# Kernel optimization log

Hardware: AMD Instinct MI355X
Metric: run time of the kernel (lower is better)

The kernel has to match this reference:

```python
import jax, jax.numpy as jnp
import numpy as np

B, HQ, S, D = 2, 16, 2048, 64   # batch, query heads, seq len, head dim
DV = 2 * D                      # value head dim (differential attention)
LAMBDA_INIT = 0.8
EPS = 1e-5
NEG = -1.0e9


def setup_inputs() -> dict:
    key = jax.random.key(0)
    ks = jax.random.split(key, 8)
    return {
        "q": jax.random.normal(ks[0], (B, HQ, S, D), dtype=jnp.float32),
        "k": jax.random.normal(ks[1], (B, HQ, S, D), dtype=jnp.float32),
        "v": jax.random.normal(ks[2], (B, HQ // 2, S, DV), dtype=jnp.float32),
        "lambda_q1": jax.random.normal(ks[3], (D,), dtype=jnp.float32) * 0.1,
        "lambda_k1": jax.random.normal(ks[4], (D,), dtype=jnp.float32) * 0.1,
        "lambda_q2": jax.random.normal(ks[5], (D,), dtype=jnp.float32) * 0.1,
        "lambda_k2": jax.random.normal(ks[6], (D,), dtype=jnp.float32) * 0.1,
        "gn_weight": jnp.ones((HQ * D,), dtype=jnp.float32),
        "gn_bias": jnp.zeros((HQ * D,), dtype=jnp.float32),
    }


def ghostmax(scores):
    # softmax with an implicit extra zero logit per row
    m = jnp.maximum(jnp.max(scores, axis=-1, keepdims=True), 0.0)
    e = jnp.exp(scores - m)
    return e / (jnp.sum(e, axis=-1, keepdims=True) + jnp.exp(-m))


def group_norm(x, weight, bias, num_groups, eps):
    # x: [B, C, S]; normalize each group over (C/G, S) like nn.GroupNorm
    b, c, s = x.shape
    xg = x.reshape(b, num_groups, (c // num_groups) * s)
    mean = jnp.mean(xg, axis=-1, keepdims=True)
    var = jnp.var(xg, axis=-1, keepdims=True)
    xn = ((xg - mean) * jax.lax.rsqrt(var + eps)).reshape(b, c, s)
    return xn * weight[None, :, None] + bias[None, :, None]


def reference(q, k, v, lambda_q1, lambda_k1, lambda_q2, lambda_k2, gn_weight, gn_bias):
    scale = 1.0 / np.sqrt(D).astype(np.float32)
    scores = jnp.einsum("bhqd,bhkd->bhqk", q, k) * scale
    causal = jnp.triu(jnp.full((S, S), NEG, dtype=scores.dtype), k=1)
    scores = scores + causal[None, None]
    w = ghostmax(scores)                                   # [B, HQ, S, S]
    w = w.reshape(B, HQ // 2, 2, S, S)
    lam1 = jnp.exp(jnp.sum(lambda_q1 * lambda_k1))
    lam2 = jnp.exp(jnp.sum(lambda_q2 * lambda_k2))
    lam = lam1 - lam2 + LAMBDA_INIT
    w = w[:, :, 0] - lam * w[:, :, 1]                      # [B, HQ/2, S, S]
    out = jnp.einsum("bhqk,bhkd->bhqd", w, v)              # [B, HQ/2, S, DV]
    out = out.reshape(B, HQ * D, S)                        # faithful to torch reshape
    out = group_norm(out, gn_weight, gn_bias, num_groups=HQ, eps=EPS)
    return out * (1.0 - LAMBDA_INIT)
```

## Files before the change

### kernel.cpp

```cpp
#include <hip/hip_runtime.h>
#include <hip/hip_bf16.h>

constexpr int B_ = 2, HQ_ = 16, HP_ = 8, S_ = 2048, D_ = 64, DV_ = 128;
constexpr float LAMB0 = 0.8f;
constexpr float EPSV = 1e-5f;

constexpr int TQ = 64, TK = 32;
constexpr int KSTR = 72;
constexpr int VSTR = 40;

typedef __attribute__((ext_vector_type(8))) short bf16x8;
typedef __attribute__((ext_vector_type(4))) float f32x4;
typedef __attribute__((ext_vector_type(4))) short short4v;

__device__ __forceinline__ unsigned short f2bf(float x) {
  unsigned u = __float_as_uint(x);
  u += 0x7FFFu + ((u >> 16) & 1u);
  return (unsigned short)(u >> 16);
}
__device__ __forceinline__ float bf2f(unsigned short h) {
  return __uint_as_float((unsigned)h << 16);
}
__device__ __forceinline__ unsigned pack2(unsigned short a, unsigned short b) {
  return (unsigned)a | ((unsigned)b << 16);
}

__launch_bounds__(256, 2)
__global__ void diffattn_fwd(const float* __restrict__ qg, const float* __restrict__ kg,
                             const float* __restrict__ vg,
                             const float* __restrict__ lq1, const float* __restrict__ lk1,
                             const float* __restrict__ lq2, const float* __restrict__ lk2,
                             float* __restrict__ Obuf) {
  __shared__ short Kl[2][2][TK][KSTR];
  __shared__ short Vt[2][DV_][VSTR];

  const int tid = threadIdx.x;
  const int w = tid >> 6;
  const int l = tid & 63;
  const int g = l >> 4;
  const int li = l & 15;

  const int t = blockIdx.x;
  const int bh = t & 15;
  const int b = bh >> 3;
  const int hp = bh & 7;
  const int u = t >> 4;
  const int qt = (u & 1) ? (31 - (u >> 1)) : (u >> 1);
  const int q0 = qt * TQ;
  const int qw = q0 + w * 16;

  float d1 = 0.f, d2 = 0.f;
  for (int i = 0; i < D_; ++i) { d1 += lq1[i] * lk1[i]; d2 += lq2[i] * lk2[i]; }
  const float lam = __expf(d1) - __expf(d2) + LAMB0;

  bf16x8 qhi[2][2], qlo[2][2];
#pragma unroll
  for (int h = 0; h < 2; ++h)
#pragma unroll
    for (int c = 0; c < 2; ++c) {
      const float* p = qg + (((size_t)b * HQ_ + 2 * hp + h) * S_ + qw + li) * D_ + c * 32 + g * 8;
      float4 a = *reinterpret_cast<const float4*>(p);
      float4 bq = *reinterpret_cast<const float4*>(p + 4);
      float xs[8] = {a.x, a.y, a.z, a.w, bq.x, bq.y, bq.z, bq.w};
      union { bf16x8 v; unsigned us[4]; } H, L;
#pragma unroll
      for (int j = 0; j < 4; ++j) {
        unsigned short h0 = f2bf(xs[2 * j]), h1 = f2bf(xs[2 * j + 1]);
        H.us[j] = pack2(h0, h1);
        L.us[j] = pack2(f2bf(xs[2 * j] - bf2f(h0)), f2bf(xs[2 * j + 1] - bf2f(h1)));
      }
      qhi[h][c] = H.v;
      qlo[h][c] = L.v;
    }

  float mreg[2] = {0.f, 0.f};
  float lreg[2] = {1.f, 1.f};
  const f32x4 zero4 = {0.f, 0.f, 0.f, 0.f};
  f32x4 Oacc[2][8];
#pragma unroll
  for (int h = 0; h < 2; ++h)
#pragma unroll
    for (int d = 0; d < 8; ++d) Oacc[h][d] = zero4;

  const int khs = tid >> 7;
  const int ktf = tid & 127;
  const float* kb0 = kg + ((size_t)b * HQ_ + 2 * hp + khs) * S_ * D_;
  const int vdv = tid & 127;
  const int vkq0 = tid >> 7;
  const float* vb0 = vg + ((size_t)b * HP_ + hp) * S_ * DV_ + vdv;

  const int nkt = (q0 + TQ) / TK;
  for (int kt = 0; kt < nkt; ++kt) {
    const int k0 = kt * TK;
    __syncthreads();

    {
      const float* kb = kb0 + (size_t)k0 * D_;
#pragma unroll
      for (int it = 0; it < 4; ++it) {
        int f = ktf + 128 * it;
        int row = f >> 4, c4 = (f & 15) * 4;
        float4 x = *reinterpret_cast<const float4*>(kb + row * D_ + c4);
        unsigned short h0 = f2bf(x.x), h1 = f2bf(x.y), h2 = f2bf(x.z), h3 = f2bf(x.w);
        short4v hi = {(short)h0, (short)h1, (short)h2, (short)h3};
        short4v lo = {(short)f2bf(x.x - bf2f(h0)), (short)f2bf(x.y - bf2f(h1)),
                      (short)f2bf(x.z - bf2f(h2)), (short)f2bf(x.w - bf2f(h3))};
        *reinterpret_cast<short4v*>(&Kl[khs][0][row][c4]) = hi;
        *reinterpret_cast<short4v*>(&Kl[khs][1][row][c4]) = lo;
      }
    }
    {
      const float* vb = vb0 + (size_t)k0 * DV_;
#pragma unroll
      for (int it = 0; it < 4; ++it) {
        int kq = vkq0 + 2 * it;
        float x0 = vb[(size_t)(kq * 4 + 0) * DV_];
        float x1 = vb[(size_t)(kq * 4 + 1) * DV_];
        float x2 = vb[(size_t)(kq * 4 + 2) * DV_];
        float x3 = vb[(size_t)(kq * 4 + 3) * DV_];
        unsigned short h0 = f2bf(x0), h1 = f2bf(x1), h2 = f2bf(x2), h3 = f2bf(x3);
        short4v hi = {(short)h0, (short)h1, (short)h2, (short)h3};
        short4v lo = {(short)f2bf(x0 - bf2f(h0)), (short)f2bf(x1 - bf2f(h1)),
                      (short)f2bf(x2 - bf2f(h2)), (short)f2bf(x3 - bf2f(h3))};
        *reinterpret_cast<short4v*>(&Vt[0][vdv][kq * 4]) = hi;
        *reinterpret_cast<short4v*>(&Vt[1][vdv][kq * 4]) = lo;
      }
    }
    __syncthreads();

    if (k0 > qw + 15) continue;
    const bool needmask = (k0 + TK - 1 > qw);

    bf16x8 Ahi[2], Alo[2];

#pragma unroll
    for (int h = 0; h < 2; ++h) {
      bf16x8 kf[2][2][2];
#pragma unroll
      for (int hl = 0; hl < 2; ++hl)
#pragma unroll
        for (int ms = 0; ms < 2; ++ms)
#pragma unroll
          for (int c = 0; c < 2; ++c)
            kf[hl][ms][c] =
                *reinterpret_cast<const bf16x8*>(&Kl[h][hl][ms * 16 + li][c * 32 + g * 8]);

      f32x4 sT[2] = {zero4, zero4};
      __builtin_amdgcn_s_setprio(1);
#pragma unroll
      for (int ms = 0; ms < 2; ++ms)
#pragma unroll
        for (int c = 0; c < 2; ++c) {
          sT[ms] = __builtin_amdgcn_mfma_f32_16x16x32_bf16(kf[0][ms][c], qhi[h][c], sT[ms], 0, 0, 0);
          sT[ms] = __builtin_amdgcn_mfma_f32_16x16x32_bf16(kf[0][ms][c], qlo[h][c], sT[ms], 0, 0, 0);
          sT[ms] = __builtin_amdgcn_mfma_f32_16x16x32_bf16(kf[1][ms][c], qhi[h][c], sT[ms], 0, 0, 0);
        }
      __builtin_amdgcn_s_setprio(0);

      const int qglob = qw + li;
      float sv[2][4];
#pragma unroll
      for (int ms = 0; ms < 2; ++ms)
#pragma unroll
        for (int r = 0; r < 4; ++r) {
          float v = sT[ms][r] * 0.125f;
          if (needmask && (k0 + ms * 16 + g * 4 + r > qglob)) v = -1e30f;
          sv[ms][r] = v;
        }
      float tmax = fmaxf(fmaxf(fmaxf(sv[0][0], sv[0][1]), fmaxf(sv[0][2], sv[0][3])),
                         fmaxf(fmaxf(sv[1][0], sv[1][1]), fmaxf(sv[1][2], sv[1][3])));
      tmax = fmaxf(tmax, __shfl_xor(tmax, 16));
      tmax = fmaxf(tmax, __shfl_xor(tmax, 32));
      const float mnew = fmaxf(mreg[h], tmax);
      const float fh = __expf(mreg[h] - mnew);
      float p[2][4];
      float psum = 0.f;
#pragma unroll
      for (int ms = 0; ms < 2; ++ms)
#pragma unroll
        for (int r = 0; r < 4; ++r) {
          p[ms][r] = __expf(sv[ms][r] - mnew);
          psum += p[ms][r];
        }
      psum += __shfl_xor(psum, 16);
      psum += __shfl_xor(psum, 32);
      lreg[h] = lreg[h] * fh + psum;
      mreg[h] = mnew;
      if (!__all(fh == 1.0f)) {
        float fr[4];
#pragma unroll
        for (int r = 0; r < 4; ++r) fr[r] = __shfl(fh, 20 * g + r);
#pragma unroll
        for (int d = 0; d < 8; ++d) {
          f32x4 o = Oacc[h][d];
          o[0] *= fr[0]; o[1] *= fr[1]; o[2] *= fr[2]; o[3] *= fr[3];
          Oacc[h][d] = o;
        }
      }

      unsigned ph0a = pack2(f2bf(p[0][0]), f2bf(p[0][1]));
      unsigned ph0b = pack2(f2bf(p[0][2]), f2bf(p[0][3]));
      unsigned ph1a = pack2(f2bf(p[1][0]), f2bf(p[1][1]));
      unsigned ph1b = pack2(f2bf(p[1][2]), f2bf(p[1][3]));
      float pl[2][4];
#pragma unroll
      for (int ms = 0; ms < 2; ++ms)
#pragma unroll
        for (int r = 0; r < 4; ++r) pl[ms][r] = p[ms][r] - bf2f(f2bf(p[ms][r]));
      unsigned pl0a = pack2(f2bf(pl[0][0]), f2bf(pl[0][1]));
      unsigned pl0b = pack2(f2bf(pl[0][2]), f2bf(pl[0][3]));
      unsigned pl1a = pack2(f2bf(pl[1][0]), f2bf(pl[1][1]));
      unsigned pl1b = pack2(f2bf(pl[1][2]), f2bf(pl[1][3]));

      const int srcA = 32 * (g & 1) + li;
      const int srcB = srcA + 16;
      const bool hiMs = (g >> 1) != 0;
      union { bf16x8 v; unsigned us[4]; } AH, AL;
      {
        unsigned a0 = (unsigned)__shfl((int)ph0a, srcA), b0 = (unsigned)__shfl((int)ph1a, srcA);
        unsigned a1 = (unsigned)__shfl((int)ph0b, srcA), b1 = (unsigned)__shfl((int)ph1b, srcA);
        unsigned a2 = (unsigned)__shfl((int)ph0a, srcB), b2 = (unsigned)__shfl((int)ph1a, srcB);
        unsigned a3 = (unsigned)__shfl((int)ph0b, srcB), b3 = (unsigned)__shfl((int)ph1b, srcB);
        AH.us[0] = hiMs ? b0 : a0; AH.us[1] = hiMs ? b1 : a1;
        AH.us[2] = hiMs ? b2 : a2; AH.us[3] = hiMs ? b3 : a3;
      }
      {
        unsigned a0 = (unsigned)__shfl((int)pl0a, srcA), b0 = (unsigned)__shfl((int)pl1a, srcA);
        unsigned a1 = (unsigned)__shfl((int)pl0b, srcA), b1 = (unsigned)__shfl((int)pl1b, srcA);
        unsigned a2 = (unsigned)__shfl((int)pl0a, srcB), b2 = (unsigned)__shfl((int)pl1a, srcB);
        unsigned a3 = (unsigned)__shfl((int)pl0b, srcB), b3 = (unsigned)__shfl((int)pl1b, srcB);
        AL.us[0] = hiMs ? b0 : a0; AL.us[1] = hiMs ? b1 : a1;
        AL.us[2] = hiMs ? b2 : a2; AL.us[3] = hiMs ? b3 : a3;
      }
      Ahi[h] = AH.v;
      Alo[h] = AL.v;
    }

    __builtin_amdgcn_s_setprio(1);
#pragma unroll
    for (int dvt = 0; dvt < 8; ++dvt) {
      bf16x8 vh = *reinterpret_cast<const bf16x8*>(&Vt[0][dvt * 16 + li][g * 8]);
      bf16x8 vl = *reinterpret_cast<const bf16x8*>(&Vt[1][dvt * 16 + li][g * 8]);
#pragma unroll
      for (int h = 0; h < 2; ++h) {
        f32x4 acc = Oacc[h][dvt];
        acc = __builtin_amdgcn_mfma_f32_16x16x32_bf16(Ahi[h], vh, acc, 0, 0, 0);
        acc = __builtin_amdgcn_mfma_f32_16x16x32_bf16(Alo[h], vh, acc, 0, 0, 0);
        acc = __builtin_amdgcn_mfma_f32_16x16x32_bf16(Ahi[h], vl, acc, 0, 0, 0);
        Oacc[h][dvt] = acc;
      }
    }
    __builtin_amdgcn_s_setprio(0);
  }

  float rl0[4], rl1[4];
#pragma unroll
  for (int r = 0; r < 4; ++r) {
    rl0[r] = 1.f / __shfl(lreg[0], 20 * g + r);
    rl1[r] = lam / __shfl(lreg[1], 20 * g + r);
  }
  float* ob = Obuf + ((size_t)(b * HP_ + hp)) * S_ * DV_;
#pragma unroll
  for (int dvt = 0; dvt < 8; ++dvt)
#pragma unroll
    for (int r = 0; r < 4; ++r) {
      float vres = Oacc[0][dvt][r] * rl0[r] - Oacc[1][dvt][r] * rl1[r];
      ob[(size_t)(qw + g * 4 + r) * DV_ + dvt * 16 + li] = vres;
    }
}

__global__ void gn_stats(const float* __restrict__ O, float* __restrict__ stats) {
  const int g = blockIdx.x >> 3;
  const int slice = blockIdx.x & 7;
  const size_t base = (size_t)g * 131072 + (size_t)slice * 16384;
  const int tid = threadIdx.x;
  float sum = 0.f, ss = 0.f;
#pragma unroll 4
  for (int it = 0; it < 16; ++it) {
    int idx = it * 256 + tid;
    float4 x = *reinterpret_cast<const float4*>(O + base + (size_t)idx * 4);
    sum += x.x + x.y + x.z + x.w;
    ss += x.x * x.x + x.y * x.y + x.z * x.z + x.w * x.w;
  }
#pragma unroll
  for (int o = 1; o < 64; o <<= 1) {
    sum += __shfl_xor(sum, o);
    ss += __shfl_xor(ss, o);
  }
  __shared__ float red[8];
  if ((tid & 63) == 0) {
    red[(tid >> 6) * 2] = sum;
    red[(tid >> 6) * 2 + 1] = ss;
  }
  __syncthreads();
  if (tid == 0) {
    atomicAdd(&stats[2 * g + 0], red[0] + red[2] + red[4] + red[6]);
    atomicAdd(&stats[2 * g + 1], red[1] + red[3] + red[5] + red[7]);
  }
}

__global__ void gn_apply(const float* __restrict__ O, const float* __restrict__ stats,
                         const float* __restrict__ gw, const float* __restrict__ gb,
                         float* __restrict__ out) {
  const size_t f = ((size_t)blockIdx.x * 256 + threadIdx.x) * 4;
  const int g = (int)(f >> 17);
  const int sidx = (int)((f >> 7) & 2047);
  const int hp = (int)((f >> 18) & 7);
  const int c = hp * 128 + (sidx >> 4);
  const float mean = stats[2 * g + 0] * (1.f / 131072.f);
  const float var = stats[2 * g + 1] * (1.f / 131072.f) - mean * mean;
  const float sc = rsqrtf(var + EPSV) * gw[c] * 0.2f;
  const float bi = gb[c] * 0.2f;
  float4 x = *reinterpret_cast<const float4*>(O + f);
  float4 y;
  y.x = (x.x - mean) * sc + bi;
  y.y = (x.y - mean) * sc + bi;
  y.z = (x.z - mean) * sc + bi;
  y.w = (x.w - mean) * sc + bi;
  *reinterpret_cast<float4*>(out + f) = y;
}

extern "C" void kernel_launch(void* const* d_in, const int* in_sizes, int n_in,
                              void* d_out, int out_size, void* d_ws, size_t ws_size,
                              hipStream_t stream) {
  const float* q = (const float*)d_in[0];
  const float* k = (const float*)d_in[1];
  const float* v = (const float*)d_in[2];
  const float* lq1 = (const float*)d_in[3];
  const float* lk1 = (const float*)d_in[4];
  const float* lq2 = (const float*)d_in[5];
  const float* lk2 = (const float*)d_in[6];
  const float* gw = (const float*)d_in[7];
  const float* gb = (const float*)d_in[8];
  float* out = (float*)d_out;

  float* Obuf = (float*)d_ws;
  float* stats = (float*)((char*)d_ws + (size_t)B_ * HP_ * S_ * DV_ * sizeof(float));

  hipMemsetAsync(stats, 0, 32 * 2 * sizeof(float), stream);
  diffattn_fwd<<<dim3(512), dim3(256), 0, stream>>>(q, k, v, lq1, lk1, lq2, lk2, Obuf);
  gn_stats<<<dim3(256), dim3(256), 0, stream>>>(Obuf, stats);
  gn_apply<<<dim3(4096), dim3(256), 0, stream>>>(Obuf, stats, gw, gb, out);
}
```

Measured before the change: 321.0 us.

## Double-buffer K/V tiles with register prefetch, lazy softmax rescale, wider gn_stats grid

The attention kernel now double-buffers the K and V shared-memory tiles. It loads the next tile's fp32 data into registers before computing on the current tile, then converts and stores it to the other buffer afterwards, so only one barrier is needed per iteration. This is meant to hide global load latency behind the MFMA work. The softmax for both heads is interleaved, and the running-max rescale now happens only when the new tile max exceeds the stored max by more than 8. That skips most accumulator rescaling, at the cost of possibly larger unnormalized values. Separately, gn_stats uses four times as many blocks, each doing less work, which adds more atomics. Register pressure rises from the prefetch buffers and the doubled LDS usage.

```diff
diff --git a/kernel.cpp b/kernel.cpp
--- a/kernel.cpp
+++ b/kernel.cpp
@@ -31,8 +31,8 @@
                              const float* __restrict__ lq1, const float* __restrict__ lk1,
                              const float* __restrict__ lq2, const float* __restrict__ lk2,
                              float* __restrict__ Obuf) {
-  __shared__ short Kl[2][2][TK][KSTR];
-  __shared__ short Vt[2][DV_][VSTR];
+  __shared__ short Kl[2][2][2][TK][KSTR];
+  __shared__ short Vt[2][2][DV_][VSTR];
 
   const int tid = threadIdx.x;
   const int w = tid >> 6;
@@ -89,168 +89,218 @@
   const int vkq0 = tid >> 7;
   const float* vb0 = vg + ((size_t)b * HP_ + hp) * S_ * DV_ + vdv;
 
+  float4 kreg[4];
+  float vreg[16];
+
+  auto issue_loads = [&](int k0) {
+    const float* kb = kb0 + (size_t)k0 * D_;
+#pragma unroll
+    for (int it = 0; it < 4; ++it) {
+      int f = ktf + 128 * it;
+      kreg[it] = *reinterpret_cast<const float4*>(kb + (f >> 4) * D_ + (f & 15) * 4);
+    }
+    const float* vb = vb0 + (size_t)k0 * DV_;
+#pragma unroll
+    for (int it = 0; it < 4; ++it) {
+      int kq = vkq0 + 2 * it;
+#pragma unroll
+      for (int c = 0; c < 4; ++c) vreg[it * 4 + c] = vb[(size_t)(kq * 4 + c) * DV_];
+    }
+  };
+
+  auto cvt_write = [&](int bufp) {
+#pragma unroll
+    for (int it = 0; it < 4; ++it) {
+      int f = ktf + 128 * it;
+      int row = f >> 4, c4 = (f & 15) * 4;
+      float4 x = kreg[it];
+      unsigned short h0 = f2bf(x.x), h1 = f2bf(x.y), h2 = f2bf(x.z), h3 = f2bf(x.w);
+      short4v hi = {(short)h0, (short)h1, (short)h2, (short)h3};
+      short4v lo = {(short)f2bf(x.x - bf2f(h0)), (short)f2bf(x.y - bf2f(h1)),
+                    (short)f2bf(x.z - bf2f(h2)), (short)f2bf(x.w - bf2f(h3))};
+      *reinterpret_cast<short4v*>(&Kl[bufp][khs][0][row][c4]) = hi;
+      *reinterpret_cast<short4v*>(&Kl[bufp][khs][1][row][c4]) = lo;
+    }
+#pragma unroll
+    for (int it = 0; it < 4; ++it) {
+      int kq = vkq0 + 2 * it;
+      float x0 = vreg[it * 4 + 0], x1 = vreg[it * 4 + 1];
+      float x2 = vreg[it * 4 + 2], x3 = vreg[it * 4 + 3];
+      unsigned short h0 = f2bf(x0), h1 = f2bf(x1), h2 = f2bf(x2), h3 = f2bf(x3);
+      short4v hi = {(short)h0, (short)h1, (short)h2, (short)h3};
+      short4v lo = {(short)f2bf(x0 - bf2f(h0)), (short)f2bf(x1 - bf2f(h1)),
+                    (short)f2bf(x2 - bf2f(h2)), (short)f2bf(x3 - bf2f(h3))};
+      *reinterpret_cast<short4v*>(&Vt[bufp][0][vdv][kq * 4]) = hi;
+      *reinterpret_cast<short4v*>(&Vt[bufp][1][vdv][kq * 4]) = lo;
+    }
+  };
+
   const int nkt = (q0 + TQ) / TK;
+
+  issue_loads(0);
+  cvt_write(0);
+  __syncthreads();
+
   for (int kt = 0; kt < nkt; ++kt) {
     const int k0 = kt * TK;
-    __syncthreads();
-
-    {
-      const float* kb = kb0 + (size_t)k0 * D_;
-#pragma unroll
-      for (int it = 0; it < 4; ++it) {
-        int f = ktf + 128 * it;
-        int row = f >> 4, c4 = (f & 15) * 4;
-        float4 x = *reinterpret_cast<const float4*>(kb + row * D_ + c4);
-        unsigned short h0 = f2bf(x.x), h1 = f2bf(x.y), h2 = f2bf(x.z), h3 = f2bf(x.w);
-        short4v hi = {(short)h0, (short)h1, (short)h2, (short)h3};
-        short4v lo = {(short)f2bf(x.x - bf2f(h0)), (short)f2bf(x.y - bf2f(h1)),
-                      (short)f2bf(x.z - bf2f(h2)), (short)f2bf(x.w - bf2f(h3))};
-        *reinterpret_cast<short4v*>(&Kl[khs][0][row][c4]) = hi;
-        *reinterpret_cast<short4v*>(&Kl[khs][1][row][c4]) = lo;
-      }
-    }
-    {
-      const float* vb = vb0 + (size_t)k0 * DV_;
-#pragma unroll
-      for (int it = 0; it < 4; ++it) {
-        int kq = vkq0 + 2 * it;
-        float x0 = vb[(size_t)(kq * 4 + 0) * DV_];
-        float x1 = vb[(size_t)(kq * 4 + 1) * DV_];
-        float x2 = vb[(size_t)(kq * 4 + 2) * DV_];
-        float x3 = vb[(size_t)(kq * 4 + 3) * DV_];
-        unsigned short h0 = f2bf(x0), h1 = f2bf(x1), h2 = f2bf(x2), h3 = f2bf(x3);
-        short4v hi = {(short)h0, (short)h1, (short)h2, (short)h3};
-        short4v lo = {(short)f2bf(x0 - bf2f(h0)), (short)f2bf(x1 - bf2f(h1)),
-                      (short)f2bf(x2 - bf2f(h2)), (short)f2bf(x3 - bf2f(h3))};
-        *reinterpret_cast<short4v*>(&Vt[0][vdv][kq * 4]) = hi;
-        *reinterpret_cast<short4v*>(&Vt[1][vdv][kq * 4]) = lo;
-      }
-    }
-    __syncthreads();
-
-    if (k0 > qw + 15) continue;
-    const bool needmask = (k0 + TK - 1 > qw);
-
-    bf16x8 Ahi[2], Alo[2];
-
-#pragma unroll
-    for (int h = 0; h < 2; ++h) {
-      bf16x8 kf[2][2][2];
-#pragma unroll
-      for (int hl = 0; hl < 2; ++hl)
+    const int p_ = kt & 1;
+
+    if (kt + 1 < nkt) issue_loads((kt + 1) * TK);
+
+    if (k0 <= qw + 15) {
+      const bool needmask = (k0 + TK - 1 > qw);
+
+      f32x4 sT[2][2];
+#pragma unroll
+      for (int h = 0; h < 2; ++h) {
+        bf16x8 kf[2][2][2];
+#pragma unroll
+        for (int hl = 0; hl < 2; ++hl)
+#pragma unroll
+          for (int ms = 0; ms < 2; ++ms)
+#pragma unroll
+            for (int c = 0; c < 2; ++c)
+              kf[hl][ms][c] = *reinterpret_cast<const bf16x8*>(
+                  &Kl[p_][h][hl][ms * 16 + li][c * 32 + g * 8]);
+        sT[h][0] = zero4;
+        sT[h][1] = zero4;
+        __builtin_amdgcn_s_setprio(1);
 #pragma unroll
         for (int ms = 0; ms < 2; ++ms)
 #pragma unroll
-          for (int c = 0; c < 2; ++c)
-            kf[hl][ms][c] =
-                *reinterpret_cast<const bf16x8*>(&Kl[h][hl][ms * 16 + li][c * 32 + g * 8]);
-
-      f32x4 sT[2] = {zero4, zero4};
-      __builtin_amdgcn_s_setprio(1);
-#pragma unroll
-      for (int ms = 0; ms < 2; ++ms)
-#pragma unroll
-        for (int c = 0; c < 2; ++c) {
-          sT[ms] = __builtin_amdgcn_mfma_f32_16x16x32_bf16(kf[0][ms][c], qhi[h][c], sT[ms], 0, 0, 0);
-          sT[ms] = __builtin_amdgcn_mfma_f32_16x16x32_bf16(kf[0][ms][c], qlo[h][c], sT[ms], 0, 0, 0);
-          sT[ms] = __builtin_amdgcn_mfma_f32_16x16x32_bf16(kf[1][ms][c], qhi[h][c], sT[ms], 0, 0, 0);
-        }
-      __builtin_amdgcn_s_setprio(0);
+          for (int c = 0; c < 2; ++c) {
+            sT[h][ms] = __builtin_amdgcn_mfma_f32_16x16x32_bf16(kf[0][ms][c], qhi[h][c], sT[h][ms], 0, 0, 0);
+            sT[h][ms] = __builtin_amdgcn_mfma_f32_16x16x32_bf16(kf[0][ms][c], qlo[h][c], sT[h][ms], 0, 0, 0);
+            sT[h][ms] = __builtin_amdgcn_mfma_f32_16x16x32_bf16(kf[1][ms][c], qhi[h][c], sT[h][ms], 0, 0, 0);
+          }
+        __builtin_amdgcn_s_setprio(0);
+      }
 
       const int qglob = qw + li;
-      float sv[2][4];
-#pragma unroll
-      for (int ms = 0; ms < 2; ++ms)
-#pragma unroll
-        for (int r = 0; r < 4; ++r) {
-          float v = sT[ms][r] * 0.125f;
-          if (needmask && (k0 + ms * 16 + g * 4 + r > qglob)) v = -1e30f;
-          sv[ms][r] = v;
-        }
-      float tmax = fmaxf(fmaxf(fmaxf(sv[0][0], sv[0][1]), fmaxf(sv[0][2], sv[0][3])),
-                         fmaxf(fmaxf(sv[1][0], sv[1][1]), fmaxf(sv[1][2], sv[1][3])));
-      tmax = fmaxf(tmax, __shfl_xor(tmax, 16));
-      tmax = fmaxf(tmax, __shfl_xor(tmax, 32));
-      const float mnew = fmaxf(mreg[h], tmax);
-      const float fh = __expf(mreg[h] - mnew);
-      float p[2][4];
-      float psum = 0.f;
-#pragma unroll
-      for (int ms = 0; ms < 2; ++ms)
-#pragma unroll
-        for (int r = 0; r < 4; ++r) {
-          p[ms][r] = __expf(sv[ms][r] - mnew);
-          psum += p[ms][r];
-        }
-      psum += __shfl_xor(psum, 16);
-      psum += __shfl_xor(psum, 32);
-      lreg[h] = lreg[h] * fh + psum;
-      mreg[h] = mnew;
-      if (!__all(fh == 1.0f)) {
-        float fr[4];
-#pragma unroll
-        for (int r = 0; r < 4; ++r) fr[r] = __shfl(fh, 20 * g + r);
-#pragma unroll
-        for (int d = 0; d < 8; ++d) {
-          f32x4 o = Oacc[h][d];
-          o[0] *= fr[0]; o[1] *= fr[1]; o[2] *= fr[2]; o[3] *= fr[3];
-          Oacc[h][d] = o;
-        }
-      }
-
-      unsigned ph0a = pack2(f2bf(p[0][0]), f2bf(p[0][1]));
-      unsigned ph0b = pack2(f2bf(p[0][2]), f2bf(p[0][3]));
-      unsigned ph1a = pack2(f2bf(p[1][0]), f2bf(p[1][1]));
-      unsigned ph1b = pack2(f2bf(p[1][2]), f2bf(p[1][3]));
-      float pl[2][4];
-#pragma unroll
-      for (int ms = 0; ms < 2; ++ms)
-#pragma unroll
-        for (int r = 0; r < 4; ++r) pl[ms][r] = p[ms][r] - bf2f(f2bf(p[ms][r]));
-      unsigned pl0a = pack2(f2bf(pl[0][0]), f2bf(pl[0][1]));
-      unsigned pl0b = pack2(f2bf(pl[0][2]), f2bf(pl[0][3]));
-      unsigned pl1a = pack2(f2bf(pl[1][0]), f2bf(pl[1][1]));
-      unsigned pl1b = pack2(f2bf(pl[1][2]), f2bf(pl[1][3]));
-
+      float sv[2][2][4];
+#pragma unroll
+      for (int h = 0; h < 2; ++h)
+#pragma unroll
+        for (int ms = 0; ms < 2; ++ms)
+#pragma unroll
+          for (int r = 0; r < 4; ++r) {
+            float v = sT[h][ms][r] * 0.125f;
+            if (needmask && (k0 + ms * 16 + g * 4 + r > qglob)) v = -1e30f;
+            sv[h][ms][r] = v;
+          }
+      float tmax[2];
+#pragma unroll
+      for (int h = 0; h < 2; ++h)
+        tmax[h] = fmaxf(fmaxf(fmaxf(sv[h][0][0], sv[h][0][1]), fmaxf(sv[h][0][2], sv[h][0][3])),
+                        fmaxf(fmaxf(sv[h][1][0], sv[h][1][1]), fmaxf(sv[h][1][2], sv[h][1][3])));
+#pragma unroll
+      for (int h = 0; h < 2; ++h) tmax[h] = fmaxf(tmax[h], __shfl_xor(tmax[h], 16));
+#pragma unroll
+      for (int h = 0; h < 2; ++h) tmax[h] = fmaxf(tmax[h], __shfl_xor(tmax[h], 32));
+
+      if (__any((tmax[0] > mreg[0] + 8.f) | (tmax[1] > mreg[1] + 8.f))) {
+        float fh[2];
+#pragma unroll
+        for (int h = 0; h < 2; ++h) {
+          const float mnew = fmaxf(mreg[h], tmax[h]);
+          fh[h] = __expf(mreg[h] - mnew);
+          mreg[h] = mnew;
+          lreg[h] *= fh[h];
+        }
+#pragma unroll
+        for (int h = 0; h < 2; ++h) {
+          float fr[4];
+#pragma unroll
+          for (int r = 0; r < 4; ++r) fr[r] = __shfl(fh[h], 20 * g + r);
+#pragma unroll
+          for (int d = 0; d < 8; ++d) {
+            f32x4 o = Oacc[h][d];
+            o[0] *= fr[0]; o[1] *= fr[1]; o[2] *= fr[2]; o[3] *= fr[3];
+            Oacc[h][d] = o;
+          }
+        }
+      }
+
+      float p[2][2][4], psum[2];
+#pragma unroll
+      for (int h = 0; h < 2; ++h) {
+        psum[h] = 0.f;
+#pragma unroll
+        for (int ms = 0; ms < 2; ++ms)
+#pragma unroll
+          for (int r = 0; r < 4; ++r) {
+            p[h][ms][r] = __expf(sv[h][ms][r] - mreg[h]);
+            psum[h] += p[h][ms][r];
+          }
+      }
+#pragma unroll
+      for (int h = 0; h < 2; ++h) psum[h] += __shfl_xor(psum[h], 16);
+#pragma unroll
+      for (int h = 0; h < 2; ++h) psum[h] += __shfl_xor(psum[h], 32);
+#pragma unroll
+      for (int h = 0; h < 2; ++h) lreg[h] += psum[h];
+
+      bf16x8 Ahi[2], Alo[2];
       const int srcA = 32 * (g & 1) + li;
       const int srcB = srcA + 16;
       const bool hiMs = (g >> 1) != 0;
-      union { bf16x8 v; unsigned us[4]; } AH, AL;
-      {
-        unsigned a0 = (unsigned)__shfl((int)ph0a, srcA), b0 = (unsigned)__shfl((int)ph1a, srcA);
-        unsigned a1 = (unsigned)__shfl((int)ph0b, srcA), b1 = (unsigned)__shfl((int)ph1b, srcA);
-        unsigned a2 = (unsigned)__shfl((int)ph0a, srcB), b2 = (unsigned)__shfl((int)ph1a, srcB);
-        unsigned a3 = (unsigned)__shfl((int)ph0b, srcB), b3 = (unsigned)__shfl((int)ph1b, srcB);
-        AH.us[0] = hiMs ? b0 : a0; AH.us[1] = hiMs ? b1 : a1;
-        AH.us[2] = hiMs ? b2 : a2; AH.us[3] = hiMs ? b3 : a3;
-      }
-      {
-        unsigned a0 = (unsigned)__shfl((int)pl0a, srcA), b0 = (unsigned)__shfl((int)pl1a, srcA);
-        unsigned a1 = (unsigned)__shfl((int)pl0b, srcA), b1 = (unsigned)__shfl((int)pl1b, srcA);
-        unsigned a2 = (unsigned)__shfl((int)pl0a, srcB), b2 = (unsigned)__shfl((int)pl1a, srcB);
-        unsigned a3 = (unsigned)__shfl((int)pl0b, srcB), b3 = (unsigned)__shfl((int)pl1b, srcB);
-        AL.us[0] = hiMs ? b0 : a0; AL.us[1] = hiMs ? b1 : a1;
-        AL.us[2] = hiMs ? b2 : a2; AL.us[3] = hiMs ? b3 : a3;
-      }
-      Ahi[h] = AH.v;
-      Alo[h] = AL.v;
-    }
-
-    __builtin_amdgcn_s_setprio(1);
-#pragma unroll
-    for (int dvt = 0; dvt < 8; ++dvt) {
-      bf16x8 vh = *reinterpret_cast<const bf16x8*>(&Vt[0][dvt * 16 + li][g * 8]);
-      bf16x8 vl = *reinterpret_cast<const bf16x8*>(&Vt[1][dvt * 16 + li][g * 8]);
 #pragma unroll
       for (int h = 0; h < 2; ++h) {
-        f32x4 acc = Oacc[h][dvt];
-        acc = __builtin_amdgcn_mfma_f32_16x16x32_bf16(Ahi[h], vh, acc, 0, 0, 0);
-        acc = __builtin_amdgcn_mfma_f32_16x16x32_bf16(Alo[h], vh, acc, 0, 0, 0);
-        acc = __builtin_amdgcn_mfma_f32_16x16x32_bf16(Ahi[h], vl, acc, 0, 0, 0);
-        Oacc[h][dvt] = acc;
-      }
-    }
-    __builtin_amdgcn_s_setprio(0);
+        unsigned ph0a = pack2(f2bf(p[h][0][0]), f2bf(p[h][0][1]));
+        unsigned ph0b = pack2(f2bf(p[h][0][2]), f2bf(p[h][0][3]));
+        unsigned ph1a = pack2(f2bf(p[h][1][0]), f2bf(p[h][1][1]));
+        unsigned ph1b = pack2(f2bf(p[h][1][2]), f2bf(p[h][1][3]));
+        float pl[2][4];
+#pragma unroll
+        for (int ms = 0; ms < 2; ++ms)
+#pragma unroll
+          for (int r = 0; r < 4; ++r) pl[ms][r] = p[h][ms][r] - bf2f(f2bf(p[h][ms][r]));
+        unsigned pl0a = pack2(f2bf(pl[0][0]), f2bf(pl[0][1]));
+        unsigned pl0b = pack2(f2bf(pl[0][2]), f2bf(pl[0][3]));
+        unsigned pl1a = pack2(f2bf(pl[1][0]), f2bf(pl[1][1]));
+        unsigned pl1b = pack2(f2bf(pl[1][2]), f2bf(pl[1][3]));
+        union { bf16x8 v; unsigned us[4]; } AH, AL;
+        {
+          unsigned a0 = (unsigned)__shfl((int)ph0a, srcA), b0 = (unsigned)__shfl((int)ph1a, srcA);
+          unsigned a1 = (unsigned)__shfl((int)ph0b, srcA), b1 = (unsigned)__shfl((int)ph1b, srcA);
+          unsigned a2 = (unsigned)__shfl((int)ph0a, srcB), b2 = (unsigned)__shfl((int)ph1a, srcB);
+          unsigned a3 = (unsigned)__shfl((int)ph0b, srcB), b3 = (unsigned)__shfl((int)ph1b, srcB);
+          AH.us[0] = hiMs ? b0 : a0; AH.us[1] = hiMs ? b1 : a1;
+          AH.us[2] = hiMs ? b2 : a2; AH.us[3] = hiMs ? b3 : a3;
+        }
+        {
+          unsigned a0 = (unsigned)__shfl((int)pl0a, srcA), b0 = (unsigned)__shfl((int)pl1a, srcA);
+          unsigned a1 = (unsigned)__shfl((int)pl0b, srcA), b1 = (unsigned)__shfl((int)pl1b, srcA);
+          unsigned a2 = (unsigned)__shfl((int)pl0a, srcB), b2 = (unsigned)__shfl((int)pl1a, srcB);
+          unsigned a3 = (unsigned)__shfl((int)pl0b, srcB), b3 = (unsigned)__shfl((int)pl1b, srcB);
+          AL.us[0] = hiMs ? b0 : a0; AL.us[1] = hiMs ? b1 : a1;
+          AL.us[2] = hiMs ? b2 : a2; AL.us[3] = hiMs ? b3 : a3;
+        }
+        Ahi[h] = AH.v;
+        Alo[h] = AL.v;
+      }
+
+      __builtin_amdgcn_s_setprio(1);
+#pragma unroll
+      for (int dvt = 0; dvt < 8; ++dvt) {
+        bf16x8 vh = *reinterpret_cast<const bf16x8*>(&Vt[p_][0][dvt * 16 + li][g * 8]);
+        bf16x8 vl = *reinterpret_cast<const bf16x8*>(&Vt[p_][1][dvt * 16 + li][g * 8]);
+#pragma unroll
+        for (int h = 0; h < 2; ++h) {
+          f32x4 acc = Oacc[h][dvt];
+          acc = __builtin_amdgcn_mfma_f32_16x16x32_bf16(Ahi[h], vh, acc, 0, 0, 0);
+          acc = __builtin_amdgcn_mfma_f32_16x16x32_bf16(Alo[h], vh, acc, 0, 0, 0);
+          acc = __builtin_amdgcn_mfma_f32_16x16x32_bf16(Ahi[h], vl, acc, 0, 0, 0);
+          Oacc[h][dvt] = acc;
+        }
+      }
+      __builtin_amdgcn_s_setprio(0);
+    }
+
+    if (kt + 1 < nkt) {
+      cvt_write((kt + 1) & 1);
+      __syncthreads();
+    }
   }
 
   float rl0[4], rl1[4];
@@ -270,13 +320,13 @@
 }
 
 __global__ void gn_stats(const float* __restrict__ O, float* __restrict__ stats) {
-  const int g = blockIdx.x >> 3;
-  const int slice = blockIdx.x & 7;
-  const size_t base = (size_t)g * 131072 + (size_t)slice * 16384;
+  const int g = blockIdx.x >> 5;
+  const int slice = blockIdx.x & 31;
+  const size_t base = (size_t)g * 131072 + (size_t)slice * 4096;
   const int tid = threadIdx.x;
   float sum = 0.f, ss = 0.f;
-#pragma unroll 4
-  for (int it = 0; it < 16; ++it) {
+#pragma unroll
+  for (int it = 0; it < 4; ++it) {
     int idx = it * 256 + tid;
     float4 x = *reinterpret_cast<const float4*>(O + base + (size_t)idx * 4);
     sum += x.x + x.y + x.z + x.w;
@@ -339,6 +389,6 @@
 
   hipMemsetAsync(stats, 0, 32 * 2 * sizeof(float), stream);
   diffattn_fwd<<<dim3(512), dim3(256), 0, stream>>>(q, k, v, lq1, lk1, lq2, lk2, Obuf);
-  gn_stats<<<dim3(256), dim3(256), 0, stream>>>(Obuf, stats);
+  gn_stats<<<dim3(1024), dim3(256), 0, stream>>>(Obuf, stats);
   gn_apply<<<dim3(4096), dim3(256), 0, stream>>>(Obuf, stats, gw, gb, out);
 }
```

New measurement: 309.2 us. 1.04x faster.
